# Kernel tuning notes

Hardware: AMD Instinct MI355X
Metric: run time of the kernel (lower is better)

## Reference

```python
import jax, jax.numpy as jnp
import numpy as np

NEG_SLOPE = 0.01  # torch LeakyReLU default
MIN_FREQ = 1.0
MAX_FREQ = 10.0
W = 100
N_HIDDEN = 100
N_OBS = 64

def _leaky(x):
    return jnp.where(x >= 0, x, NEG_SLOPE * x)

def setup_inputs() -> dict:
    key = jax.random.key(0)
    ks = jax.random.split(key, 7)
    # kaiming_uniform-ish init scales (exact init doesn't matter for correctness baseline)
    def unif(k, shape, fan_in):
        bound = np.sqrt(6.0 / fan_in)
        return jax.random.uniform(k, shape, jnp.float32, -bound, bound)
    x = jax.random.normal(ks[0], (65536, N_OBS), jnp.float32)
    W_in = unif(ks[1], (N_OBS, W), N_OBS)
    b_in = jnp.zeros((W,), jnp.float32)
    Ws = unif(ks[2], (N_HIDDEN, W, W), W)
    bs = jnp.zeros((N_HIDDEN, W), jnp.float32)
    W_out = unif(ks[3], (W, 1), W)
    b_out = jnp.zeros((1,), jnp.float32)
    return {"x": x, "W_in": W_in, "b_in": b_in, "Ws": Ws, "bs": bs,
            "W_out": W_out, "b_out": b_out}

def reference(x, W_in, b_in, Ws, bs, W_out, b_out):
    h = _leaky(x @ W_in + b_in)                       # [B, 100]
    def layer(h, wb):
        w, b = wb
        return _leaky(h @ w + b), None
    h, _ = jax.lax.scan(layer, h, (Ws, bs))           # 100 hidden layers
    a = h @ W_out + b_out                             # [B, 1]
    a = jnp.tanh(a)
    return (a + 1.0) / 2.0 * (MAX_FREQ - MIN_FREQ) + MIN_FREQ
```

## Files before the change

kernel.cpp:

```cpp
#include <hip/hip_runtime.h>
#include <cmath>

#define NLAYERS 100
#define DIN     64
#define WDIM    100
#define NTT     4
#define RT      2
#define ROWS    64
#define KS      7

typedef _Float16 half8  __attribute__((ext_vector_type(8)));
typedef _Float16 half2v __attribute__((ext_vector_type(2)));
typedef __fp16   fp16x2 __attribute__((ext_vector_type(2)));
typedef float    f32x4  __attribute__((ext_vector_type(4)));
typedef float    f32x16 __attribute__((ext_vector_type(16)));
typedef unsigned uint4v __attribute__((ext_vector_type(4)));

#define WSH_LAYER_HALVES (KS * NTT * 64 * 8)
#define WSH_HALVES       (NLAYERS * WSH_LAYER_HALVES)
#define W0_HALVES        (4 * NTT * 64 * 8)
#define BPAD_FLOATS      128
#define OFF_BPAD_B       ((WSH_HALVES + W0_HALVES) * 2)
#define OFF_WOUT_B       (OFF_BPAD_B + BPAD_FLOATS * 4)
#define WOUT_FLOATS      128

__global__ __launch_bounds__(256)
void actor_prep(const float* __restrict__ Win, const float* __restrict__ bin,
                const float* __restrict__ Ws,  const float* __restrict__ bs,
                const float* __restrict__ Wout,
                _Float16* __restrict__ wsh, _Float16* __restrict__ w0sh,
                float* __restrict__ bpad, float* __restrict__ woutp) {
    __shared__ float tile[16 * 128];
    const int bid = blockIdx.x, tid = threadIdx.x;
    if (bid < NLAYERS * KS) {
        const int l = bid / KS, ks = bid % KS;
#pragma unroll
        for (int e = 0; e < 8; ++e) {
            int idx = tid + 256 * e;
            int kk = idx >> 7, nn = idx & 127;
            int k = ks * 16 + kk;
            float v = 0.f;
            if (k < WDIM && nn < WDIM)        v = Ws[(l * WDIM + k) * WDIM + nn];
            else if (k == WDIM && nn < WDIM)  v = bs[l * WDIM + nn];
            else if (k == WDIM && nn == WDIM) v = 1.0f;
            tile[idx] = v;
        }
        __syncthreads();
        const int lane = tid & 63, nt = tid >> 6;
        const int g = lane >> 5, n = nt * 32 + (lane & 31);
        half8 o;
#pragma unroll
        for (int j = 0; j < 8; ++j) o[j] = (_Float16)tile[(g * 8 + j) * 128 + n];
        *(half8*)(wsh + (((l * KS + ks) * NTT + nt) << 9) + lane * 8) = o;
        return;
    }
    int b2 = bid - NLAYERS * KS;
    if (b2 < 4) {
        const int ks = b2;
#pragma unroll
        for (int e = 0; e < 8; ++e) {
            int idx = tid + 256 * e;
            int kk = idx >> 7, nn = idx & 127;
            int k = ks * 16 + kk;
            tile[idx] = (nn < WDIM) ? Win[k * WDIM + nn] : 0.f;
        }
        __syncthreads();
        const int lane = tid & 63, nt = tid >> 6;
        const int g = lane >> 5, n = nt * 32 + (lane & 31);
        half8 o;
#pragma unroll
        for (int j = 0; j < 8; ++j) o[j] = (_Float16)tile[(g * 8 + j) * 128 + n];
        *(half8*)(w0sh + ((ks * NTT + nt) << 9) + lane * 8) = o;
        return;
    }
    if (tid < BPAD_FLOATS) {
        bpad[tid] = (tid < WDIM) ? bin[tid] : (tid == WDIM ? 1.0f : 0.f);
    } else {
        int t = tid - BPAD_FLOATS;
        if (t < WOUT_FLOATS) woutp[t] = (t < WDIM) ? Wout[t] : 0.f;
    }
}

__device__ __forceinline__ void split8(const float* __restrict__ p, half8& hi, half8& lo) {
    f32x4 u0 = *(const f32x4*)p;
    f32x4 u1 = *(const f32x4*)(p + 4);
    float v[8] = {u0[0], u0[1], u0[2], u0[3], u1[0], u1[1], u1[2], u1[3]};
#pragma unroll
    for (int e = 0; e < 8; e += 2) {
        fp16x2 h = __builtin_amdgcn_cvt_pkrtz(v[e], v[e + 1]);
        float r0 = v[e]     - (float)h[0];
        float r1 = v[e + 1] - (float)h[1];
        fp16x2 l = __builtin_amdgcn_cvt_pkrtz(r0, r1);
        hi[e] = (_Float16)h[0]; hi[e + 1] = (_Float16)h[1];
        lo[e] = (_Float16)l[0]; lo[e + 1] = (_Float16)l[1];
    }
}

__device__ __forceinline__ unsigned pack2(float a, float b) {
    half2v p; p[0] = (_Float16)a; p[1] = (_Float16)b;
    const half2v slope = {(_Float16)0.01f, (_Float16)0.01f};
    p = __builtin_elementwise_max(p, p * slope);
    return __builtin_bit_cast(unsigned, p);
}

__global__ __launch_bounds__(64, 1)
void actor_main(const float* __restrict__ x,
                const _Float16* __restrict__ wsh,
                const _Float16* __restrict__ w0sh,
                const float* __restrict__ bpad,
                const float* __restrict__ woutp,
                const float* __restrict__ bout,
                float* __restrict__ out) {
    const int lane = threadIdx.x;
    const int g = lane >> 5, b31 = lane & 31;
    const int rowbase = blockIdx.x * ROWS;

    f32x16 acc[RT][NTT];
    half8 wb[KS][NTT];
    half8 bh[RT][KS];
    const f32x16 zero16 = {0,0,0,0, 0,0,0,0, 0,0,0,0, 0,0,0,0};

    {
        half8 w0[4][NTT];
#pragma unroll
        for (int ks = 0; ks < 4; ++ks)
#pragma unroll
            for (int nt = 0; nt < NTT; ++nt)
                w0[ks][nt] = *(const half8*)(w0sh + (ks * NTT + nt) * 512 + lane * 8);
#pragma unroll
        for (int rt = 0; rt < RT; ++rt)
#pragma unroll
            for (int nt = 0; nt < NTT; ++nt)
#pragma unroll
                for (int qd = 0; qd < 4; ++qd) {
                    f32x4 tq = *(const f32x4*)(bpad + nt * 32 + 8 * qd + 4 * g);
#pragma unroll
                    for (int r = 0; r < 4; ++r) acc[rt][nt][4 * qd + r] = tq[r];
                }
#pragma unroll
        for (int rt = 0; rt < RT; ++rt) {
            const float* xr = x + (rowbase + rt * 32 + b31) * DIN;
#pragma unroll
            for (int ks = 0; ks < 4; ++ks) {
                half8 xhi, xlo;
                split8(xr + ks * 16 + g * 8, xhi, xlo);
#pragma unroll
                for (int nt = 0; nt < NTT; ++nt) {
                    acc[rt][nt] = __builtin_amdgcn_mfma_f32_32x32x16_f16(w0[ks][nt], xhi, acc[rt][nt], 0, 0, 0);
                    acc[rt][nt] = __builtin_amdgcn_mfma_f32_32x32x16_f16(w0[ks][nt], xlo, acc[rt][nt], 0, 0, 0);
                }
            }
        }
    }
#pragma unroll
    for (int rt = 0; rt < RT; ++rt)
#pragma unroll
        for (int ks = 0; ks < KS; ++ks) {
            const int r0 = 8 * (ks & 1);
            const f32x16 a = acc[rt][ks >> 1];
            unsigned lo0 = pack2(a[r0 + 0], a[r0 + 1]);
            unsigned lo1 = pack2(a[r0 + 2], a[r0 + 3]);
            unsigned hi0 = pack2(a[r0 + 4], a[r0 + 5]);
            unsigned hi1 = pack2(a[r0 + 6], a[r0 + 7]);
            asm volatile("v_permlane32_swap_b32 %0, %1" : "+v"(lo0), "+v"(hi0));
            asm volatile("v_permlane32_swap_b32 %0, %1" : "+v"(lo1), "+v"(hi1));
            uint4v u = {lo0, lo1, hi0, hi1};
            bh[rt][ks] = __builtin_bit_cast(half8, u);
        }
#pragma unroll
    for (int ks = 0; ks < KS; ++ks)
#pragma unroll
        for (int nt = 0; nt < NTT; ++nt)
            wb[ks][nt] = *(const half8*)(wsh + (ks * NTT + nt) * 512 + lane * 8);

#pragma unroll 1
    for (int l = 0; l < NLAYERS; ++l) {
        const _Float16* wn = wsh + (l < NLAYERS - 1 ? l + 1 : l) * WSH_LAYER_HALVES;
#pragma unroll
        for (int ks = 0; ks < KS; ++ks) {
#pragma unroll
            for (int rt = 0; rt < RT; ++rt)
#pragma unroll
                for (int nt = 0; nt < NTT; ++nt)
                    acc[rt][nt] = __builtin_amdgcn_mfma_f32_32x32x16_f16(
                        wb[ks][nt], bh[rt][ks], (ks == 0 ? zero16 : acc[rt][nt]), 0, 0, 0);
#pragma unroll
            for (int nt = 0; nt < NTT; ++nt)
                wb[ks][nt] = *(const half8*)(wn + (ks * NTT + nt) * 512 + lane * 8);
        }
        if (l < NLAYERS - 1) {
#pragma unroll
            for (int rt = 0; rt < RT; ++rt)
#pragma unroll
                for (int ks = 0; ks < KS; ++ks) {
                    const int r0 = 8 * (ks & 1);
                    const f32x16 a = acc[rt][ks >> 1];
                    unsigned lo0 = pack2(a[r0 + 0], a[r0 + 1]);
                    unsigned lo1 = pack2(a[r0 + 2], a[r0 + 3]);
                    unsigned hi0 = pack2(a[r0 + 4], a[r0 + 5]);
                    unsigned hi1 = pack2(a[r0 + 6], a[r0 + 7]);
                    asm volatile("v_permlane32_swap_b32 %0, %1" : "+v"(lo0), "+v"(hi0));
                    asm volatile("v_permlane32_swap_b32 %0, %1" : "+v"(lo1), "+v"(hi1));
                    uint4v u = {lo0, lo1, hi0, hi1};
                    bh[rt][ks] = __builtin_bit_cast(half8, u);
                }
#pragma unroll
            for (int ks = 0; ks < KS; ++ks)
#pragma unroll
                for (int nt = 0; nt < NTT; ++nt)
                    asm volatile("" : "+v"(wb[ks][nt]));
        }
    }

    float part[RT];
#pragma unroll
    for (int rt = 0; rt < RT; ++rt) {
        float s = 0.f;
#pragma unroll
        for (int nt = 0; nt < NTT; ++nt)
#pragma unroll
            for (int qd = 0; qd < 4; ++qd) {
                f32x4 w4 = *(const f32x4*)(woutp + nt * 32 + 8 * qd + 4 * g);
#pragma unroll
                for (int r = 0; r < 4; ++r) {
                    float a = acc[rt][nt][4 * qd + r];
                    float v = fmaxf(a, 0.01f * a);
                    s += v * w4[r];
                }
            }
        s += __shfl_xor(s, 32);
        part[rt] = s;
    }
    if (lane < 32) {
#pragma unroll
        for (int rt = 0; rt < RT; ++rt) {
            float tot = part[rt] + bout[0];
            out[rowbase + rt * 32 + b31] = tanhf(tot) * 4.5f + 5.5f;
        }
    }
}

extern "C" void kernel_launch(void* const* d_in, const int* in_sizes, int n_in,
                              void* d_out, int out_size, void* d_ws, size_t ws_size,
                              hipStream_t stream) {
    const float* x    = (const float*)d_in[0];
    const float* Win  = (const float*)d_in[1];
    const float* bin  = (const float*)d_in[2];
    const float* Ws   = (const float*)d_in[3];
    const float* bs   = (const float*)d_in[4];
    const float* Wout = (const float*)d_in[5];
    const float* bout = (const float*)d_in[6];
    float* out = (float*)d_out;

    char* ws = (char*)d_ws;
    _Float16* wsh  = (_Float16*)ws;
    _Float16* w0sh = wsh + WSH_HALVES;
    float* bpad  = (float*)(ws + OFF_BPAD_B);
    float* woutp = (float*)(ws + OFF_WOUT_B);

    hipLaunchKernelGGL(actor_prep, dim3(NLAYERS * KS + 4 + 1), dim3(256), 0, stream,
                       Win, bin, Ws, bs, Wout, wsh, w0sh, bpad, woutp);

    const int nrows = in_sizes[0] / DIN;
    hipLaunchKernelGGL(actor_main, dim3(nrows / ROWS), dim3(64), 0, stream,
                       x, wsh, w0sh, bpad, woutp, bout, out);
}
```

Before: 256.3 us.

## Double-buffer layer weights in registers with prefetch two layers ahead

Keeps two register sets of weight fragments and unrolls the layer loop by two, so the weights for layer l+2 load while layers l and l+1 compute. This gives global loads a full extra layer of MFMA work to hide their latency, instead of fetching only the next layer. In exchange it roughly doubles weight register usage, which risks spills or scheduling pressure. It also drops the asm barriers that pinned the weight registers.

```diff
diff --git a/kernel.cpp b/kernel.cpp
--- a/kernel.cpp
+++ b/kernel.cpp
@@ -101,6 +101,43 @@
     const half2v slope = {(_Float16)0.01f, (_Float16)0.01f};
     p = __builtin_elementwise_max(p, p * slope);
     return __builtin_bit_cast(unsigned, p);
+}
+
+__device__ __forceinline__ void pack_bh(const f32x16 (&acc)[RT][NTT], half8 (&bh)[RT][KS]) {
+#pragma unroll
+    for (int rt = 0; rt < RT; ++rt)
+#pragma unroll
+        for (int ks = 0; ks < KS; ++ks) {
+            const int r0 = 8 * (ks & 1);
+            const f32x16 a = acc[rt][ks >> 1];
+            unsigned lo0 = pack2(a[r0 + 0], a[r0 + 1]);
+            unsigned lo1 = pack2(a[r0 + 2], a[r0 + 3]);
+            unsigned hi0 = pack2(a[r0 + 4], a[r0 + 5]);
+            unsigned hi1 = pack2(a[r0 + 6], a[r0 + 7]);
+            asm volatile("v_permlane32_swap_b32 %0, %1" : "+v"(lo0), "+v"(hi0));
+            asm volatile("v_permlane32_swap_b32 %0, %1" : "+v"(lo1), "+v"(hi1));
+            uint4v u = {lo0, lo1, hi0, hi1};
+            bh[rt][ks] = __builtin_bit_cast(half8, u);
+        }
+}
+
+static __device__ const f32x16 kZero16 = {0,0,0,0, 0,0,0,0, 0,0,0,0, 0,0,0,0};
+
+__device__ __forceinline__ void layer_mfma(f32x16 (&acc)[RT][NTT], const half8 (&bh)[RT][KS],
+                                           half8 (&wb)[KS][NTT],
+                                           const _Float16* __restrict__ wn, int lane) {
+#pragma unroll
+    for (int ks = 0; ks < KS; ++ks) {
+#pragma unroll
+        for (int rt = 0; rt < RT; ++rt)
+#pragma unroll
+            for (int nt = 0; nt < NTT; ++nt)
+                acc[rt][nt] = __builtin_amdgcn_mfma_f32_32x32x16_f16(
+                    wb[ks][nt], bh[rt][ks], (ks == 0 ? kZero16 : acc[rt][nt]), 0, 0, 0);
+#pragma unroll
+        for (int nt = 0; nt < NTT; ++nt)
+            wb[ks][nt] = *(const half8*)(wn + (ks * NTT + nt) * 512 + lane * 8);
+    }
 }
 
 __global__ __launch_bounds__(64, 1)
@@ -116,9 +153,9 @@
     const int rowbase = blockIdx.x * ROWS;
 
     f32x16 acc[RT][NTT];
-    half8 wb[KS][NTT];
+    half8 wbA[KS][NTT];
+    half8 wbB[KS][NTT];
     half8 bh[RT][KS];
-    const f32x16 zero16 = {0,0,0,0, 0,0,0,0, 0,0,0,0, 0,0,0,0};
 
     {
         half8 w0[4][NTT];
@@ -153,63 +190,23 @@
         }
     }
 #pragma unroll
-    for (int rt = 0; rt < RT; ++rt)
-#pragma unroll
-        for (int ks = 0; ks < KS; ++ks) {
-            const int r0 = 8 * (ks & 1);
-            const f32x16 a = acc[rt][ks >> 1];
-            unsigned lo0 = pack2(a[r0 + 0], a[r0 + 1]);
-            unsigned lo1 = pack2(a[r0 + 2], a[r0 + 3]);
-            unsigned hi0 = pack2(a[r0 + 4], a[r0 + 5]);
-            unsigned hi1 = pack2(a[r0 + 6], a[r0 + 7]);
-            asm volatile("v_permlane32_swap_b32 %0, %1" : "+v"(lo0), "+v"(hi0));
-            asm volatile("v_permlane32_swap_b32 %0, %1" : "+v"(lo1), "+v"(hi1));
-            uint4v u = {lo0, lo1, hi0, hi1};
-            bh[rt][ks] = __builtin_bit_cast(half8, u);
-        }
-#pragma unroll
     for (int ks = 0; ks < KS; ++ks)
 #pragma unroll
-        for (int nt = 0; nt < NTT; ++nt)
-            wb[ks][nt] = *(const half8*)(wsh + (ks * NTT + nt) * 512 + lane * 8);
+        for (int nt = 0; nt < NTT; ++nt) {
+            wbA[ks][nt] = *(const half8*)(wsh + (ks * NTT + nt) * 512 + lane * 8);
+            wbB[ks][nt] = *(const half8*)(wsh + WSH_LAYER_HALVES + (ks * NTT + nt) * 512 + lane * 8);
+        }
+    pack_bh(acc, bh);
 
 #pragma unroll 1
-    for (int l = 0; l < NLAYERS; ++l) {
-        const _Float16* wn = wsh + (l < NLAYERS - 1 ? l + 1 : l) * WSH_LAYER_HALVES;
-#pragma unroll
-        for (int ks = 0; ks < KS; ++ks) {
-#pragma unroll
-            for (int rt = 0; rt < RT; ++rt)
-#pragma unroll
-                for (int nt = 0; nt < NTT; ++nt)
-                    acc[rt][nt] = __builtin_amdgcn_mfma_f32_32x32x16_f16(
-                        wb[ks][nt], bh[rt][ks], (ks == 0 ? zero16 : acc[rt][nt]), 0, 0, 0);
-#pragma unroll
-            for (int nt = 0; nt < NTT; ++nt)
-                wb[ks][nt] = *(const half8*)(wn + (ks * NTT + nt) * 512 + lane * 8);
-        }
-        if (l < NLAYERS - 1) {
-#pragma unroll
-            for (int rt = 0; rt < RT; ++rt)
-#pragma unroll
-                for (int ks = 0; ks < KS; ++ks) {
-                    const int r0 = 8 * (ks & 1);
-                    const f32x16 a = acc[rt][ks >> 1];
-                    unsigned lo0 = pack2(a[r0 + 0], a[r0 + 1]);
-                    unsigned lo1 = pack2(a[r0 + 2], a[r0 + 3]);
-                    unsigned hi0 = pack2(a[r0 + 4], a[r0 + 5]);
-                    unsigned hi1 = pack2(a[r0 + 6], a[r0 + 7]);
-                    asm volatile("v_permlane32_swap_b32 %0, %1" : "+v"(lo0), "+v"(hi0));
-                    asm volatile("v_permlane32_swap_b32 %0, %1" : "+v"(lo1), "+v"(hi1));
-                    uint4v u = {lo0, lo1, hi0, hi1};
-                    bh[rt][ks] = __builtin_bit_cast(half8, u);
-                }
-#pragma unroll
-            for (int ks = 0; ks < KS; ++ks)
-#pragma unroll
-                for (int nt = 0; nt < NTT; ++nt)
-                    asm volatile("" : "+v"(wb[ks][nt]));
-        }
+    for (int l = 0; l < NLAYERS; l += 2) {
+        const int lA = (l + 2 < NLAYERS) ? l + 2 : NLAYERS - 1;
+        const int lB = (l + 3 < NLAYERS) ? l + 3 : NLAYERS - 1;
+        layer_mfma(acc, bh, wbA, wsh + lA * WSH_LAYER_HALVES, lane);
+        pack_bh(acc, bh);
+        layer_mfma(acc, bh, wbB, wsh + lB * WSH_LAYER_HALVES, lane);
+        if (l + 1 < NLAYERS - 1)
+            pack_bh(acc, bh);
     }
 
     float part[RT];
```

Measured after the change: 343.5 us. +34.0%, slower.
